# Kernel optimization log

Measured on AMD Instinct MI355X. Metric: run time of the kernel, lower is better.

Reference implementation:

```python
import jax, jax.numpy as jnp
import numpy as np

B, S, H = 64, 512, 768
ATT_H, CLS_H = 100, 300


def setup_inputs() -> dict:
    key = jax.random.key(0)
    ks = jax.random.split(key, 8)
    hidden_states = jax.random.normal(ks[0], (B, S, H), jnp.float32)
    is_cont = jax.random.bernoulli(ks[1], 0.25, (B, S)).at[:, 0].set(False)
    offset_mapping = jnp.stack(
        [is_cont.astype(jnp.int32) * 3, jnp.zeros((B, S), jnp.int32)], axis=-1
    )
    labels = jax.random.randint(ks[2], (B, S), -1, 2).astype(jnp.float32)
    s = 0.02
    W1 = jax.random.normal(ks[3], (H, ATT_H), jnp.float32) * s
    b1 = jnp.zeros((ATT_H,), jnp.float32)
    W2 = jax.random.normal(ks[4], (ATT_H, 1), jnp.float32) * s
    b2 = jnp.zeros((1,), jnp.float32)
    W3 = jax.random.normal(ks[5], (H, CLS_H), jnp.float32) * s
    b3 = jnp.zeros((CLS_H,), jnp.float32)
    W4 = jax.random.normal(ks[6], (CLS_H, 1), jnp.float32) * s
    b4 = jnp.zeros((1,), jnp.float32)
    return dict(hidden_states=hidden_states, offset_mapping=offset_mapping,
                labels=labels, W1=W1, b1=b1, W2=W2, b2=b2, W3=W3, b3=b3,
                W4=W4, b4=b4)


def reference(hidden_states, offset_mapping, labels, W1, b1, W2, b2, W3, b3, W4, b4):
    beta = 1.0            # soft_attention_beta
    w_sent, w_tok, w_reg = 1.0, 1.0, 0.01
    Bn, Sn, _ = hidden_states.shape

    # token attention head: sigmoid(tanh(h W1 + b1) W2 + b2) -> [B, S]
    token_att = jax.nn.sigmoid(jnp.tanh(hidden_states @ W1 + b1) @ W2 + b2)[..., 0]

    # --- subword grouping as a single segment-max ---
    # a continuation token (offset[...,0] != 0) belongs to the segment started
    # by the previous non-continuation token (the word root).
    is_cont = offset_mapping[:, :, 0] != 0          # [B, S]
    start = jnp.logical_not(is_cont)
    start_flat = start.reshape(-1)
    seg_id = jnp.cumsum(start_flat.astype(jnp.int32)) - 1   # [B*S]
    vals = token_att.reshape(-1)
    seg_red = jax.ops.segment_max(vals, seg_id, num_segments=Bn * Sn)  # 'max' subword_method
    # scatter the group reduction back onto the word-root position only
    word_att = jnp.where(start_flat, seg_red[seg_id], vals).reshape(Bn, Sn)

    # mask: labelled (!= -1) AND not a subword continuation
    mask = (jnp.logical_and(labels != -1.0, start)).astype(hidden_states.dtype)
    masked = word_att * mask                          # token_logits

    # soft attention pooling over sequence
    p = jnp.power(masked, beta)
    norm = p / jnp.sum(p, axis=1, keepdims=True)      # [B, S]
    pooled = jnp.einsum('bsh,bs->bh', hidden_states, norm)

    sent = jax.nn.sigmoid(jnp.tanh(pooled @ W3 + b3) @ W4 + b4)  # [B, 1]

    # --- losses (_calculate_loss) ---
    sent_labels = jnp.max(labels, axis=1, keepdims=True)          # [B, 1]
    sentence_loss = jnp.sum((sent - sent_labels) ** 2)
    zero_labels = jnp.where(labels == 1.0, labels, 0.0)
    token_loss = jnp.sum((masked - zero_labels) ** 2)
    ones_mask = jnp.where(masked == 0.0, 1.0, masked)
    reg_a = jnp.sum(jnp.min(ones_mask, axis=1, keepdims=True) ** 2)
    reg_b = jnp.sum((jnp.max(masked, axis=1, keepdims=True) - sent_labels) ** 2)
    loss = w_sent * sentence_loss + w_tok * token_loss + w_reg * (reg_a + reg_b)

    return (loss, sentence_loss, token_loss, reg_a, reg_b,
            hidden_states, masked, sent)
```

## Files before the change

kernel.cpp:

```cpp
#include <hip/hip_runtime.h>
#include <math.h>

#define Bn 64
#define Sn 512
#define Hn 768
#define ATT_H 100
#define CLS_H 300
#define Mtok (Bn*Sn)
#define NP 112
#define NT 7

#define W1T_N (NP*Hn)
#define W3T_N (CLS_H*Hn)
#define NSG 16

typedef __attribute__((ext_vector_type(8))) short short8;
typedef __attribute__((ext_vector_type(4))) float floatx4;

__device__ inline float sigf(float x) { return 1.0f / (1.0f + expf(-x)); }

__device__ inline unsigned short f2bf(float x) {
    union { float f; unsigned int u; } v; v.f = x;
    unsigned int r = (v.u + 0x7FFFu + ((v.u >> 16) & 1u)) >> 16;
    return (unsigned short)r;
}

__device__ inline float wred_sum(float v) {
    #pragma unroll
    for (int d = 32; d; d >>= 1) v += __shfl_down(v, d, 64);
    return v;
}
__device__ inline float wred_max(float v) {
    #pragma unroll
    for (int d = 32; d; d >>= 1) v = fmaxf(v, __shfl_down(v, d, 64));
    return v;
}
__device__ inline float wred_min(float v) {
    #pragma unroll
    for (int d = 32; d; d >>= 1) v = fminf(v, __shfl_down(v, d, 64));
    return v;
}

__global__ __launch_bounds__(256) void k0_prep(
    const float* __restrict__ W1, const float* __restrict__ b1,
    const float* __restrict__ W2, const float* __restrict__ W3,
    unsigned short* __restrict__ w1t, float* __restrict__ b1w2,
    float* __restrict__ w3t)
{
    int idx = blockIdx.x * 256 + threadIdx.x;
    if (idx < W1T_N) {
        int lane = (idx >> 3) & 63;
        int t = idx >> 9;
        int ct = t % 7;
        int n = ct * 16 + (lane & 15);
        if (n >= ATT_H) w1t[idx] = 0;
    } else if (idx < W1T_N + Hn * ATT_H) {
        int i = idx - W1T_N;
        int k = i / ATT_H, n = i - k * ATT_H;
        int ct = n >> 4, u = n & 15;
        int kstep = k >> 5, q = (k & 31) >> 3, e = k & 7;
        w1t[((kstep * 7 + ct) * 64 + (q * 16 + u)) * 8 + e] = f2bf(W1[i]);
    } else if (idx < W1T_N + Hn * ATT_H + W3T_N) {
        int i = idx - (W1T_N + Hn * ATT_H);
        int k = i / CLS_H, j = i - k * CLS_H;
        w3t[(size_t)j * Hn + k] = W3[i];
    } else if (idx < W1T_N + Hn * ATT_H + W3T_N + NP) {
        int j = idx - (W1T_N + Hn * ATT_H + W3T_N);
        b1w2[2 * j]     = (j < ATT_H) ? b1[j] : 0.f;
        b1w2[2 * j + 1] = (j < ATT_H) ? W2[j] : 0.f;
    }
}

__global__ __launch_bounds__(256, 3) void k1_att(
    const float* __restrict__ h, const unsigned short* __restrict__ w1t,
    const float* __restrict__ b1w2, const float* __restrict__ b2,
    float* __restrict__ att)
{
    __shared__ __align__(16) char smem[32768];

    const int tid = threadIdx.x;
    const int wave = tid >> 6, lane = tid & 63;
    const int u = lane & 15, q = lane >> 4;
    const int g = wave;
    const int tok0 = blockIdx.x * 32;

    const int lr = lane >> 4;
    const int lcb = (lane & 15) * 8;

    floatx4 acc0[NT], acc1[NT];
    #pragma unroll
    for (int ct = 0; ct < NT; ct++) { acc0[ct] = (floatx4)0.f; acc1[ct] = (floatx4)0.f; }

    const short8* __restrict__ w1f = (const short8*)w1t;
    char* const sb = smem + wave * 8192;

    floatx4 v[8];
    #pragma unroll
    for (int j = 0; j < 8; j++) {
        size_t gidx = (size_t)(tok0 + j * 4 + lr) * Hn + g * 192 + lcb / 2;
        v[j] = *(const floatx4*)(h + gidx);
    }

    #pragma unroll
    for (int ch = 0; ch < 3; ch++) {
        char* stage = sb + (ch & 1) * 4096;

        #pragma unroll
        for (int j = 0; j < 8; j++) {
            int row = j * 4 + lr;
            ushort4 bv;
            bv.x = f2bf(v[j].x); bv.y = f2bf(v[j].y);
            bv.z = f2bf(v[j].z); bv.w = f2bf(v[j].w);
            *(ushort4*)(stage + row * 128 + (lcb ^ ((row & 7) << 4))) = bv;
        }

        if (ch < 2) {
            const int kbase = g * 192 + ch * 64;
            #pragma unroll
            for (int j = 0; j < 8; j++) {
                size_t gidx = (size_t)(tok0 + j * 4 + lr) * Hn + kbase + 64 + lcb / 2;
                v[j] = *(const floatx4*)(h + gidx);
            }
        }

        #pragma unroll
        for (int ks = 0; ks < 2; ks++) {
            const int kstep = g * 6 + ch * 2 + ks;
            short8 a0 = *(const short8*)(stage + u * 128
                                         + ((ks * 64 + q * 16) ^ ((u & 7) << 4)));
            short8 a1 = *(const short8*)(stage + (16 + u) * 128
                                         + ((ks * 64 + q * 16) ^ ((u & 7) << 4)));
            #pragma unroll
            for (int ct = 0; ct < NT; ct++) {
                short8 bfr = w1f[(kstep * 7 + ct) * 64 + lane];
                acc0[ct] = __builtin_amdgcn_mfma_f32_16x16x32_bf16(a0, bfr, acc0[ct], 0, 0, 0);
                acc1[ct] = __builtin_amdgcn_mfma_f32_16x16x32_bf16(a1, bfr, acc1[ct], 0, 0, 0);
            }
        }
    }

    float* cb = (float*)smem;
    __syncthreads();
    if (g > 0) {
        #pragma unroll
        for (int ct = 0; ct < NT; ct++)
            *(floatx4*)(&cb[((g - 1) * 64 + lane) * 28 + ct * 4]) = acc0[ct];
    }
    __syncthreads();
    if (g == 0) {
        #pragma unroll
        for (int o = 0; o < 3; o++)
            #pragma unroll
            for (int ct = 0; ct < NT; ct++)
                acc0[ct] += *(const floatx4*)(&cb[(o * 64 + lane) * 28 + ct * 4]);
        float z[4] = {0.f, 0.f, 0.f, 0.f};
        #pragma unroll
        for (int ct = 0; ct < NT; ct++) {
            float2 bw = *(const float2*)(b1w2 + (ct * 16 + u) * 2);
            #pragma unroll
            for (int r = 0; r < 4; r++)
                z[r] += tanhf(acc0[ct][r] + bw.x) * bw.y;
        }
        #pragma unroll
        for (int mask = 1; mask < 16; mask <<= 1) {
            #pragma unroll
            for (int r = 0; r < 4; r++) z[r] += __shfl_xor(z[r], mask, 64);
        }
        if (u == 0) {
            float bb2 = b2[0];
            #pragma unroll
            for (int r = 0; r < 4; r++)
                att[tok0 + q * 4 + r] = sigf(z[r] + bb2);
        }
    }
    __syncthreads();
    if (g > 0) {
        #pragma unroll
        for (int ct = 0; ct < NT; ct++)
            *(floatx4*)(&cb[((g - 1) * 64 + lane) * 28 + ct * 4]) = acc1[ct];
    }
    __syncthreads();
    if (g == 0) {
        #pragma unroll
        for (int o = 0; o < 3; o++)
            #pragma unroll
            for (int ct = 0; ct < NT; ct++)
                acc1[ct] += *(const floatx4*)(&cb[(o * 64 + lane) * 28 + ct * 4]);
        float z[4] = {0.f, 0.f, 0.f, 0.f};
        #pragma unroll
        for (int ct = 0; ct < NT; ct++) {
            float2 bw = *(const float2*)(b1w2 + (ct * 16 + u) * 2);
            #pragma unroll
            for (int r = 0; r < 4; r++)
                z[r] += tanhf(acc1[ct][r] + bw.x) * bw.y;
        }
        #pragma unroll
        for (int mask = 1; mask < 16; mask <<= 1) {
            #pragma unroll
            for (int r = 0; r < 4; r++) z[r] += __shfl_xor(z[r], mask, 64);
        }
        if (u == 0) {
            float bb2 = b2[0];
            #pragma unroll
            for (int r = 0; r < 4; r++)
                att[tok0 + 16 + q * 4 + r] = sigf(z[r] + bb2);
        }
    }
}

__global__ __launch_bounds__(256) void k2_seg(
    const float* __restrict__ att, const int* __restrict__ offset,
    const float* __restrict__ labels, float* __restrict__ masked_out,
    float* __restrict__ sum_m, float* __restrict__ slab_o,
    float* __restrict__ tl_o, float* __restrict__ mino_o,
    float* __restrict__ maxm_o)
{
    const int b = blockIdx.x, tid = threadIdx.x;
    __shared__ float attl[Sn];
    __shared__ int   startl[Sn];
    __shared__ float rsum[4], rtl[4], rsl[4], rmn[4], rmx[4];

    for (int s = tid; s < Sn; s += 256) {
        attl[s] = att[b * Sn + s];
        startl[s] = (offset[(size_t)(b * Sn + s) * 2] == 0) ? 1 : 0;
    }
    __syncthreads();

    float lsum = 0.f, ltl = 0.f, lslab = -1e30f, lmin = 1e30f, lmax = -1e30f;
    for (int s = tid; s < Sn; s += 256) {
        float lab = labels[b * Sn + s];
        int st = startl[s];
        float m = 0.f;
        if (st && lab != -1.0f) {
            m = attl[s];
            for (int t = s + 1; t < Sn && !startl[t]; t++)
                m = fmaxf(m, attl[t]);
        }
        masked_out[b * Sn + s] = m;
        lsum += m;
        float zl = (lab == 1.0f) ? 1.f : 0.f;
        ltl += (m - zl) * (m - zl);
        lslab = fmaxf(lslab, lab);
        float om = (m == 0.f) ? 1.f : m;
        lmin = fminf(lmin, om);
        lmax = fmaxf(lmax, m);
    }
    int wid = tid >> 6, lane = tid & 63;
    lsum = wred_sum(lsum); ltl = wred_sum(ltl);
    lslab = wred_max(lslab); lmin = wred_min(lmin); lmax = wred_max(lmax);
    if (lane == 0) { rsum[wid]=lsum; rtl[wid]=ltl; rsl[wid]=lslab; rmn[wid]=lmin; rmx[wid]=lmax; }
    __syncthreads();
    if (tid == 0) {
        sum_m[b]  = rsum[0]+rsum[1]+rsum[2]+rsum[3];
        tl_o[b]   = rtl[0]+rtl[1]+rtl[2]+rtl[3];
        slab_o[b] = fmaxf(fmaxf(rsl[0],rsl[1]), fmaxf(rsl[2],rsl[3]));
        mino_o[b] = fminf(fminf(rmn[0],rmn[1]), fminf(rmn[2],rmn[3]));
        maxm_o[b] = fmaxf(fmaxf(rmx[0],rmx[1]), fmaxf(rmx[2],rmx[3]));
    }
}

__global__ __launch_bounds__(192) void k3_pool(
    const float* __restrict__ h, const float* __restrict__ masked,
    const float* __restrict__ sum_m, float* __restrict__ part,
    float* __restrict__ out_hidden)
{
    const int b = blockIdx.x, sg = blockIdx.y;
    const int tid = threadIdx.x;
    __shared__ float nrm[32];
    if (tid < 32)
        nrm[tid] = masked[b * Sn + sg * 32 + tid] * (1.0f / sum_m[b]);
    __syncthreads();
    const size_t base = ((size_t)b * Sn + sg * 32) * Hn;
    const floatx4* hp = (const floatx4*)(h + base) + tid;
    float ax = 0.f, ay = 0.f, az = 0.f, aw = 0.f;
    #pragma unroll 8
    for (int s = 0; s < 32; s++) {
        floatx4 v = hp[(size_t)s * (Hn / 4)];
        *(floatx4*)(out_hidden + base + (size_t)s * Hn + tid * 4) = v;
        float w = nrm[s];
        ax += v.x * w; ay += v.y * w; az += v.z * w; aw += v.w * w;
    }
    floatx4 o; o.x = ax; o.y = ay; o.z = az; o.w = aw;
    *(floatx4*)(part + ((size_t)b * NSG + sg) * Hn + tid * 4) = o;
}

__global__ __launch_bounds__(256) void k4_sent(
    const float* __restrict__ part, const float* __restrict__ w3t,
    const float* __restrict__ b3, const float* __restrict__ W4,
    float* __restrict__ zpart)
{
    const int b = blockIdx.x, jc = blockIdx.y;
    const int tid = threadIdx.x;
    __shared__ __align__(16) float pl[Hn];
    __shared__ float yred[64];
    for (int k = tid; k < Hn; k += 256) {
        float s = 0.f;
        #pragma unroll
        for (int g = 0; g < NSG; g++)
            s += part[((size_t)b * NSG + g) * Hn + k];
        pl[k] = s;
    }
    if (tid < 64) yred[tid] = 0.f;
    __syncthreads();
    int jj = tid >> 2, ks = tid & 3;
    float a = 0.f;
    if (jj < 60) {
        int j = jc * 60 + jj;
        const floatx4* wr = (const floatx4*)(w3t + (size_t)j * Hn) + ks * 48;
        const floatx4* pr = (const floatx4*)pl + ks * 48;
        #pragma unroll 8
        for (int i = 0; i < 48; i++) {
            floatx4 wv = wr[i]; floatx4 pv = pr[i];
            a += wv.x * pv.x + wv.y * pv.y + wv.z * pv.z + wv.w * pv.w;
        }
    }
    a += __shfl_xor(a, 1, 64);
    a += __shfl_xor(a, 2, 64);
    if (jj < 60 && ks == 0) {
        int j = jc * 60 + jj;
        yred[jj] = tanhf(a + b3[j]) * W4[j];
    }
    __syncthreads();
    if (tid < 64) {
        float y = yred[tid];
        y = wred_sum(y);
        if (tid == 0) zpart[jc * Bn + b] = y;
    }
}

__global__ __launch_bounds__(64) void k5_loss(
    const float* __restrict__ zpart, const float* __restrict__ b4,
    const float* __restrict__ slab, const float* __restrict__ tl,
    const float* __restrict__ mino, const float* __restrict__ maxm,
    float* __restrict__ out, float* __restrict__ out_sent)
{
    int t = threadIdx.x;
    float z = b4[0];
    #pragma unroll
    for (int jc = 0; jc < 5; jc++) z += zpart[jc * Bn + t];
    float sent = sigf(z);
    out_sent[t] = sent;
    float sl = slab[t];
    float e1 = (sent - sl) * (sent - sl);
    float e2 = tl[t];
    float e3 = mino[t] * mino[t];
    float mm = maxm[t] - sl;
    float e4 = mm * mm;
    e1 = wred_sum(e1); e2 = wred_sum(e2); e3 = wred_sum(e3); e4 = wred_sum(e4);
    if (t == 0) {
        out[1] = e1;
        out[2] = e2;
        out[3] = e3;
        out[4] = e4;
        out[0] = e1 + e2 + 0.01f * (e3 + e4);
    }
}

extern "C" void kernel_launch(void* const* d_in, const int* in_sizes, int n_in,
                              void* d_out, int out_size, void* d_ws, size_t ws_size,
                              hipStream_t stream) {
    (void)in_sizes; (void)n_in; (void)out_size; (void)ws_size;
    const float* h      = (const float*)d_in[0];
    const int*   offset = (const int*)d_in[1];
    const float* labels = (const float*)d_in[2];
    const float* W1     = (const float*)d_in[3];
    const float* b1     = (const float*)d_in[4];
    const float* W2     = (const float*)d_in[5];
    const float* b2     = (const float*)d_in[6];
    const float* W3     = (const float*)d_in[7];
    const float* b3     = (const float*)d_in[8];
    const float* W4     = (const float*)d_in[9];
    const float* b4     = (const float*)d_in[10];

    float* out        = (float*)d_out;
    float* out_hidden = out + 5;
    float* out_masked = out_hidden + (size_t)Bn * Sn * Hn;
    float* out_sent   = out_masked + (size_t)Bn * Sn;

    float* ws      = (float*)d_ws;
    float* att     = ws;
    float* sum_m   = att + Mtok;
    float* slab    = sum_m + Bn;
    float* tlb     = slab + Bn;
    float* mino    = tlb + Bn;
    float* maxm    = mino + Bn;
    float* part    = maxm + Bn;
    float* zpart   = part + (size_t)Bn * NSG * Hn;
    float* b1w2    = zpart + 5 * Bn;
    float* w3t     = b1w2 + 2 * NP;
    unsigned short* w1t = (unsigned short*)(w3t + W3T_N);

    int k0_total = W1T_N + Hn * ATT_H + W3T_N + NP;
    k0_prep<<<(k0_total + 255) / 256, 256, 0, stream>>>(W1, b1, W2, W3,
                                                        w1t, b1w2, w3t);
    k1_att<<<Mtok / 32, 256, 0, stream>>>(h, w1t, b1w2, b2, att);
    k2_seg<<<Bn, 256, 0, stream>>>(att, offset, labels, out_masked,
                                   sum_m, slab, tlb, mino, maxm);
    k3_pool<<<dim3(Bn, NSG), 192, 0, stream>>>(h, out_masked, sum_m, part,
                                               out_hidden);
    k4_sent<<<dim3(Bn, 5), 256, 0, stream>>>(part, w3t, b3, W4, zpart);
    k5_loss<<<1, 64, 0, stream>>>(zpart, b4, slab, tlb, mino, maxm, out, out_sent);
}
```

Baseline: 257.3 us.

## Stage W1 through shared memory with full-K waves and fuse segment-max into pooling

The attention kernel now gives each wave 16 tokens across the full hidden dimension. It double-buffers the bf16 W1 tiles through shared memory in 12 chunks, replacing the old split-K across waves with its cross-wave LDS reduction and per-wave global W1 fetches. The segment-max/masking kernel is merged into the pooling kernel, which drops one launch and the masked/sum round trip through global memory. The cost is that each pooling block recomputes the whole 512-token segment scan redundantly (16× per batch), and occupancy drops to 2 blocks per CU.

```diff
diff --git a/kernel.cpp b/kernel.cpp
--- a/kernel.cpp
+++ b/kernel.cpp
@@ -13,6 +13,7 @@
 #define W1T_N (NP*Hn)
 #define W3T_N (CLS_H*Hn)
 #define NSG 16
+#define BCHUNK 14336
 
 typedef __attribute__((ext_vector_type(8))) short short8;
 typedef __attribute__((ext_vector_type(4))) float floatx4;
@@ -71,153 +72,131 @@
     }
 }
 
-__global__ __launch_bounds__(256, 3) void k1_att(
+__global__ __launch_bounds__(256, 2) void k1_att(
     const float* __restrict__ h, const unsigned short* __restrict__ w1t,
     const float* __restrict__ b1w2, const float* __restrict__ b2,
     float* __restrict__ att)
 {
-    __shared__ __align__(16) char smem[32768];
+    __shared__ __align__(16) char Bb[2][BCHUNK];
+    __shared__ __align__(16) char Ab[4][2][2048];
 
     const int tid = threadIdx.x;
     const int wave = tid >> 6, lane = tid & 63;
     const int u = lane & 15, q = lane >> 4;
-    const int g = wave;
-    const int tok0 = blockIdx.x * 32;
-
+    const int tokw = blockIdx.x * 64 + wave * 16;
     const int lr = lane >> 4;
     const int lcb = (lane & 15) * 8;
 
-    floatx4 acc0[NT], acc1[NT];
-    #pragma unroll
-    for (int ct = 0; ct < NT; ct++) { acc0[ct] = (floatx4)0.f; acc1[ct] = (floatx4)0.f; }
-
-    const short8* __restrict__ w1f = (const short8*)w1t;
-    char* const sb = smem + wave * 8192;
-
-    floatx4 v[8];
-    #pragma unroll
-    for (int j = 0; j < 8; j++) {
-        size_t gidx = (size_t)(tok0 + j * 4 + lr) * Hn + g * 192 + lcb / 2;
-        v[j] = *(const floatx4*)(h + gidx);
-    }
-
-    #pragma unroll
-    for (int ch = 0; ch < 3; ch++) {
-        char* stage = sb + (ch & 1) * 4096;
-
-        #pragma unroll
-        for (int j = 0; j < 8; j++) {
+    const char* __restrict__ w1b = (const char*)w1t;
+
+    floatx4 acc[NT];
+    #pragma unroll
+    for (int ct = 0; ct < NT; ct++) acc[ct] = (floatx4)0.f;
+
+    floatx4 breg[4];
+    #pragma unroll
+    for (int p = 0; p < 4; p++) {
+        int off = tid * 16 + p * 4096;
+        if (off < BCHUNK) breg[p] = *(const floatx4*)(w1b + off);
+    }
+    floatx4 v[4];
+    #pragma unroll
+    for (int j = 0; j < 4; j++)
+        v[j] = *(const floatx4*)(h + (size_t)(tokw + j * 4 + lr) * Hn
+                                 + (lane & 15) * 4);
+    #pragma unroll
+    for (int p = 0; p < 4; p++) {
+        int off = tid * 16 + p * 4096;
+        if (off < BCHUNK) *(floatx4*)(&Bb[0][off]) = breg[p];
+    }
+    #pragma unroll
+    for (int p = 0; p < 4; p++) {
+        int off = tid * 16 + p * 4096;
+        if (off < BCHUNK) breg[p] = *(const floatx4*)(w1b + BCHUNK + off);
+    }
+
+    #pragma unroll 2
+    for (int ch = 0; ch < 12; ch++) {
+        __syncthreads();
+
+        if (ch < 11) {
+            #pragma unroll
+            for (int p = 0; p < 4; p++) {
+                int off = tid * 16 + p * 4096;
+                if (off < BCHUNK) *(floatx4*)(&Bb[(ch + 1) & 1][off]) = breg[p];
+            }
+        }
+        if (ch < 10) {
+            #pragma unroll
+            for (int p = 0; p < 4; p++) {
+                int off = tid * 16 + p * 4096;
+                if (off < BCHUNK)
+                    breg[p] = *(const floatx4*)(w1b + (size_t)(ch + 2) * BCHUNK + off);
+            }
+        }
+
+        char* as = &Ab[wave][ch & 1][0];
+        #pragma unroll
+        for (int j = 0; j < 4; j++) {
             int row = j * 4 + lr;
             ushort4 bv;
             bv.x = f2bf(v[j].x); bv.y = f2bf(v[j].y);
             bv.z = f2bf(v[j].z); bv.w = f2bf(v[j].w);
-            *(ushort4*)(stage + row * 128 + (lcb ^ ((row & 7) << 4))) = bv;
-        }
-
-        if (ch < 2) {
-            const int kbase = g * 192 + ch * 64;
+            *(ushort4*)(as + row * 128 + (lcb ^ ((row & 7) << 4))) = bv;
+        }
+        if (ch < 11) {
             #pragma unroll
-            for (int j = 0; j < 8; j++) {
-                size_t gidx = (size_t)(tok0 + j * 4 + lr) * Hn + kbase + 64 + lcb / 2;
-                v[j] = *(const floatx4*)(h + gidx);
-            }
-        }
-
+            for (int j = 0; j < 4; j++)
+                v[j] = *(const floatx4*)(h + (size_t)(tokw + j * 4 + lr) * Hn
+                                         + (ch + 1) * 64 + (lane & 15) * 4);
+        }
+
+        const char* bs = &Bb[ch & 1][0];
         #pragma unroll
         for (int ks = 0; ks < 2; ks++) {
-            const int kstep = g * 6 + ch * 2 + ks;
-            short8 a0 = *(const short8*)(stage + u * 128
-                                         + ((ks * 64 + q * 16) ^ ((u & 7) << 4)));
-            short8 a1 = *(const short8*)(stage + (16 + u) * 128
-                                         + ((ks * 64 + q * 16) ^ ((u & 7) << 4)));
+            short8 a = *(const short8*)(as + u * 128
+                                        + ((ks * 64 + q * 16) ^ ((u & 7) << 4)));
             #pragma unroll
             for (int ct = 0; ct < NT; ct++) {
-                short8 bfr = w1f[(kstep * 7 + ct) * 64 + lane];
-                acc0[ct] = __builtin_amdgcn_mfma_f32_16x16x32_bf16(a0, bfr, acc0[ct], 0, 0, 0);
-                acc1[ct] = __builtin_amdgcn_mfma_f32_16x16x32_bf16(a1, bfr, acc1[ct], 0, 0, 0);
+                short8 bfr = *(const short8*)(bs + ((ks * 7 + ct) * 64 + lane) * 16);
+                acc[ct] = __builtin_amdgcn_mfma_f32_16x16x32_bf16(a, bfr, acc[ct], 0, 0, 0);
             }
         }
     }
 
-    float* cb = (float*)smem;
-    __syncthreads();
-    if (g > 0) {
-        #pragma unroll
-        for (int ct = 0; ct < NT; ct++)
-            *(floatx4*)(&cb[((g - 1) * 64 + lane) * 28 + ct * 4]) = acc0[ct];
-    }
-    __syncthreads();
-    if (g == 0) {
-        #pragma unroll
-        for (int o = 0; o < 3; o++)
-            #pragma unroll
-            for (int ct = 0; ct < NT; ct++)
-                acc0[ct] += *(const floatx4*)(&cb[(o * 64 + lane) * 28 + ct * 4]);
-        float z[4] = {0.f, 0.f, 0.f, 0.f};
-        #pragma unroll
-        for (int ct = 0; ct < NT; ct++) {
-            float2 bw = *(const float2*)(b1w2 + (ct * 16 + u) * 2);
-            #pragma unroll
-            for (int r = 0; r < 4; r++)
-                z[r] += tanhf(acc0[ct][r] + bw.x) * bw.y;
-        }
-        #pragma unroll
-        for (int mask = 1; mask < 16; mask <<= 1) {
-            #pragma unroll
-            for (int r = 0; r < 4; r++) z[r] += __shfl_xor(z[r], mask, 64);
-        }
-        if (u == 0) {
-            float bb2 = b2[0];
-            #pragma unroll
-            for (int r = 0; r < 4; r++)
-                att[tok0 + q * 4 + r] = sigf(z[r] + bb2);
-        }
-    }
-    __syncthreads();
-    if (g > 0) {
-        #pragma unroll
-        for (int ct = 0; ct < NT; ct++)
-            *(floatx4*)(&cb[((g - 1) * 64 + lane) * 28 + ct * 4]) = acc1[ct];
-    }
-    __syncthreads();
-    if (g == 0) {
-        #pragma unroll
-        for (int o = 0; o < 3; o++)
-            #pragma unroll
-            for (int ct = 0; ct < NT; ct++)
-                acc1[ct] += *(const floatx4*)(&cb[(o * 64 + lane) * 28 + ct * 4]);
-        float z[4] = {0.f, 0.f, 0.f, 0.f};
-        #pragma unroll
-        for (int ct = 0; ct < NT; ct++) {
-            float2 bw = *(const float2*)(b1w2 + (ct * 16 + u) * 2);
-            #pragma unroll
-            for (int r = 0; r < 4; r++)
-                z[r] += tanhf(acc1[ct][r] + bw.x) * bw.y;
-        }
-        #pragma unroll
-        for (int mask = 1; mask < 16; mask <<= 1) {
-            #pragma unroll
-            for (int r = 0; r < 4; r++) z[r] += __shfl_xor(z[r], mask, 64);
-        }
-        if (u == 0) {
-            float bb2 = b2[0];
-            #pragma unroll
-            for (int r = 0; r < 4; r++)
-                att[tok0 + 16 + q * 4 + r] = sigf(z[r] + bb2);
-        }
-    }
-}
-
-__global__ __launch_bounds__(256) void k2_seg(
-    const float* __restrict__ att, const int* __restrict__ offset,
-    const float* __restrict__ labels, float* __restrict__ masked_out,
-    float* __restrict__ sum_m, float* __restrict__ slab_o,
-    float* __restrict__ tl_o, float* __restrict__ mino_o,
-    float* __restrict__ maxm_o)
-{
-    const int b = blockIdx.x, tid = threadIdx.x;
+    float z[4] = {0.f, 0.f, 0.f, 0.f};
+    #pragma unroll
+    for (int ct = 0; ct < NT; ct++) {
+        float2 bw = *(const float2*)(b1w2 + (ct * 16 + u) * 2);
+        #pragma unroll
+        for (int r = 0; r < 4; r++)
+            z[r] += tanhf(acc[ct][r] + bw.x) * bw.y;
+    }
+    #pragma unroll
+    for (int mask = 1; mask < 16; mask <<= 1) {
+        #pragma unroll
+        for (int r = 0; r < 4; r++) z[r] += __shfl_xor(z[r], mask, 64);
+    }
+    if (u == 0) {
+        float bb2 = b2[0];
+        #pragma unroll
+        for (int r = 0; r < 4; r++)
+            att[tokw + q * 4 + r] = sigf(z[r] + bb2);
+    }
+}
+
+__global__ __launch_bounds__(256) void k3_pool(
+    const float* __restrict__ h, const float* __restrict__ att,
+    const int* __restrict__ offset, const float* __restrict__ labels,
+    float* __restrict__ masked_out, float* __restrict__ part,
+    float* __restrict__ out_hidden,
+    float* __restrict__ slab_o, float* __restrict__ tl_o,
+    float* __restrict__ mino_o, float* __restrict__ maxm_o)
+{
+    const int b = blockIdx.x, sg = blockIdx.y, tid = threadIdx.x;
     __shared__ float attl[Sn];
     __shared__ int   startl[Sn];
+    __shared__ float ml[Sn];
     __shared__ float rsum[4], rtl[4], rsl[4], rmn[4], rmx[4];
 
     for (int s = tid; s < Sn; s += 256) {
@@ -233,10 +212,10 @@
         float m = 0.f;
         if (st && lab != -1.0f) {
             m = attl[s];
-            for (int t = s + 1; t < Sn && !startl[t]; t++)
-                m = fmaxf(m, attl[t]);
-        }
-        masked_out[b * Sn + s] = m;
+            for (int t2 = s + 1; t2 < Sn && !startl[t2]; t2++)
+                m = fmaxf(m, attl[t2]);
+        }
+        ml[s] = m;
         lsum += m;
         float zl = (lab == 1.0f) ? 1.f : 0.f;
         ltl += (m - zl) * (m - zl);
@@ -250,38 +229,32 @@
     lslab = wred_max(lslab); lmin = wred_min(lmin); lmax = wred_max(lmax);
     if (lane == 0) { rsum[wid]=lsum; rtl[wid]=ltl; rsl[wid]=lslab; rmn[wid]=lmin; rmx[wid]=lmax; }
     __syncthreads();
-    if (tid == 0) {
-        sum_m[b]  = rsum[0]+rsum[1]+rsum[2]+rsum[3];
-        tl_o[b]   = rtl[0]+rtl[1]+rtl[2]+rtl[3];
-        slab_o[b] = fmaxf(fmaxf(rsl[0],rsl[1]), fmaxf(rsl[2],rsl[3]));
-        mino_o[b] = fminf(fminf(rmn[0],rmn[1]), fminf(rmn[2],rmn[3]));
-        maxm_o[b] = fmaxf(fmaxf(rmx[0],rmx[1]), fmaxf(rmx[2],rmx[3]));
-    }
-}
-
-__global__ __launch_bounds__(192) void k3_pool(
-    const float* __restrict__ h, const float* __restrict__ masked,
-    const float* __restrict__ sum_m, float* __restrict__ part,
-    float* __restrict__ out_hidden)
-{
-    const int b = blockIdx.x, sg = blockIdx.y;
-    const int tid = threadIdx.x;
-    __shared__ float nrm[32];
-    if (tid < 32)
-        nrm[tid] = masked[b * Sn + sg * 32 + tid] * (1.0f / sum_m[b]);
-    __syncthreads();
-    const size_t base = ((size_t)b * Sn + sg * 32) * Hn;
-    const floatx4* hp = (const floatx4*)(h + base) + tid;
-    float ax = 0.f, ay = 0.f, az = 0.f, aw = 0.f;
-    #pragma unroll 8
-    for (int s = 0; s < 32; s++) {
-        floatx4 v = hp[(size_t)s * (Hn / 4)];
-        *(floatx4*)(out_hidden + base + (size_t)s * Hn + tid * 4) = v;
-        float w = nrm[s];
-        ax += v.x * w; ay += v.y * w; az += v.z * w; aw += v.w * w;
-    }
-    floatx4 o; o.x = ax; o.y = ay; o.z = az; o.w = aw;
-    *(floatx4*)(part + ((size_t)b * NSG + sg) * Hn + tid * 4) = o;
+
+    if (sg == 0) {
+        if (tid == 0) {
+            tl_o[b]   = rtl[0]+rtl[1]+rtl[2]+rtl[3];
+            slab_o[b] = fmaxf(fmaxf(rsl[0],rsl[1]), fmaxf(rsl[2],rsl[3]));
+            mino_o[b] = fminf(fminf(rmn[0],rmn[1]), fminf(rmn[2],rmn[3]));
+            maxm_o[b] = fmaxf(fmaxf(rmx[0],rmx[1]), fmaxf(rmx[2],rmx[3]));
+        }
+        for (int s = tid; s < Sn; s += 256) masked_out[b * Sn + s] = ml[s];
+    }
+
+    float inv = 1.0f / (rsum[0]+rsum[1]+rsum[2]+rsum[3]);
+    if (tid < 192) {
+        const size_t base = ((size_t)b * Sn + sg * 32) * Hn;
+        const floatx4* hp = (const floatx4*)(h + base) + tid;
+        float ax = 0.f, ay = 0.f, az = 0.f, aw = 0.f;
+        #pragma unroll 8
+        for (int s = 0; s < 32; s++) {
+            floatx4 vv = hp[(size_t)s * (Hn / 4)];
+            *(floatx4*)(out_hidden + base + (size_t)s * Hn + tid * 4) = vv;
+            float w = ml[sg * 32 + s] * inv;
+            ax += vv.x * w; ay += vv.y * w; az += vv.z * w; aw += vv.w * w;
+        }
+        floatx4 o; o.x = ax; o.y = ay; o.z = az; o.w = aw;
+        *(floatx4*)(part + ((size_t)b * NSG + sg) * Hn + tid * 4) = o;
+    }
 }
 
 __global__ __launch_bounds__(256) void k4_sent(
@@ -393,11 +366,10 @@
     int k0_total = W1T_N + Hn * ATT_H + W3T_N + NP;
     k0_prep<<<(k0_total + 255) / 256, 256, 0, stream>>>(W1, b1, W2, W3,
                                                         w1t, b1w2, w3t);
-    k1_att<<<Mtok / 32, 256, 0, stream>>>(h, w1t, b1w2, b2, att);
-    k2_seg<<<Bn, 256, 0, stream>>>(att, offset, labels, out_masked,
-                                   sum_m, slab, tlb, mino, maxm);
-    k3_pool<<<dim3(Bn, NSG), 192, 0, stream>>>(h, out_masked, sum_m, part,
-                                               out_hidden);
+    k1_att<<<Mtok / 64, 256, 0, stream>>>(h, w1t, b1w2, b2, att);
+    k3_pool<<<dim3(Bn, NSG), 256, 0, stream>>>(h, att, offset, labels,
+                                               out_masked, part, out_hidden,
+                                               slab, tlb, mino, maxm);
     k4_sent<<<dim3(Bn, 5), 256, 0, stream>>>(part, w3t, b3, W4, zpart);
     k5_loss<<<1, 64, 0, stream>>>(zpart, b4, slab, tlb, mino, maxm, out, out_sent);
 }
```

New measurement: 248.5 us. -3.4%, faster.
